# Optimization experiments

Measured on AMD Instinct MI355X. Metric: run time of the kernel, lower is better.

## Reference

```python
import jax, jax.numpy as jnp
import numpy as np

TASK_WEIGHT = 1.0
PHYSICS_WEIGHT = 0.3
HZ = 50.0


def physics_scores(w, hz=HZ):
    """Vectorized port of _score_window_raw. w: [B, T, 3] float. Assumes T >= 20.
    Returns float32 [B] scores in {0, 55..90}."""
    w = jax.lax.stop_gradient(w)  # torch version detaches via .cpu().item()
    B, T, _ = w.shape
    n = T
    mean = jnp.mean(w, axis=1, keepdims=True)          # [B,1,3]
    d = w - mean                                        # centered
    tv = jnp.sum(d * d, axis=(1, 2)) / n                # [B] total (biased) variance
    reject = tv < 0.005
    # per-axis saturation check: too many samples pinned at max |value|
    absw = jnp.abs(w)                                   # [B,T,3]
    max_val = jnp.max(absw, axis=1)                     # [B,3]
    at_max_frac = jnp.mean(jnp.abs(absw - max_val[:, None, :]) < 0.01, axis=1)  # [B,3]
    reject |= jnp.any((max_val >= 0.5) & (at_max_frac > 0.2), axis=1)
    # jerk law (hz >= 50): central-difference twice, p95 of |jerk| pooled over axes
    if hz >= 50:
        dt = 1.0 / hz
        vel = (w[:, 2:, :] - w[:, :-2, :]) / (2 * dt)       # [B, T-2, 3]
        jerk = (vel[:, 2:, :] - vel[:, :-2, :]) / (2 * dt)  # [B, T-4, 3]
        jerks = jnp.abs(jerk).reshape(B, -1)                # [B, 3*(T-4)]
        js = jnp.sort(jerks, axis=1)
        p95_idx = int(jerks.shape[1] * 0.95)                # matches jerks[int(len*0.95)]
        reject |= js[:, p95_idx] > 5000
    # variance-tier score
    s1 = jnp.where(tv > 10.0, 90.0,
         jnp.where(tv > 2.0, 80.0,
         jnp.where(tv > 0.5, 70.0, 58.0)))
    # zero-crossing rate of centered x-axis
    dx = d[:, :, 0]                                      # [B,T]
    zcr = jnp.sum(dx[:, 1:] * dx[:, :-1] < 0, axis=1) / n
    s2 = jnp.where(zcr > 0.15, 85.0, jnp.where(zcr > 0.07, 70.0, 55.0))
    score = jnp.floor((s1 + s2) / 2.0)                   # int() truncation (values positive)
    return jnp.where(reject, 0.0, score).astype(jnp.float32)


def setup_inputs() -> dict:
    key = jax.random.key(0)
    k1, k2, k3 = jax.random.split(key, 3)
    B, T, C = 32768, 512, 128
    predictions = jax.random.normal(k1, (B, C), dtype=jnp.float32)
    labels = jax.random.randint(k2, (B,), 0, C, dtype=jnp.int64)
    # scale accel so physics checks pass with realistic-looking noise (std 0.1 m/s^2)
    imu_windows = 0.1 * jax.random.normal(k3, (B, T, 3), dtype=jnp.float32)
    return {"predictions": predictions, "labels": labels, "imu_windows": imu_windows}


def reference(predictions, labels, imu_windows):
    # task loss: mean cross-entropy
    logp = jax.nn.log_softmax(predictions, axis=-1)                      # [B,C]
    task_loss = -jnp.mean(jnp.take_along_axis(logp, labels[:, None], axis=1)[:, 0])
    # physics penalty
    scores = physics_scores(imu_windows, HZ)                             # [B]
    physics_penalty = jnp.mean(1.0 - scores / 100.0)
    return TASK_WEIGHT * task_loss + PHYSICS_WEIGHT * physics_penalty
```

## Files before the change

kernel.cpp:

```cpp
#include <hip/hip_runtime.h>
#include <math.h>

__device__ __forceinline__ float wave_reduce_sum(float v) {
#pragma unroll
    for (int off = 32; off > 0; off >>= 1) v += __shfl_xor(v, off, 64);
    return v;
}
__device__ __forceinline__ float wave_reduce_max(float v) {
#pragma unroll
    for (int off = 32; off > 0; off >>= 1) v = fmaxf(v, __shfl_xor(v, off, 64));
    return v;
}
__device__ __forceinline__ int wave_reduce_sum_i(int v) {
#pragma unroll
    for (int off = 32; off > 0; off >>= 1) v += __shfl_xor(v, off, 64);
    return v;
}

template <int CT_C>
__global__ void ce_kernel(const float* __restrict__ preds,
                          const int* __restrict__ labels,
                          float* __restrict__ partials, int B, int C_rt) {
    __shared__ float sh[4];
    const int wave = threadIdx.x >> 6, lane = threadIdx.x & 63;
    const int row = blockIdx.x * 4 + wave;
    float loss = 0.f;
    if (row < B) {
        const int C = (CT_C > 0) ? CT_C : C_rt;
        constexpr int NV = (CT_C > 0) ? (CT_C / 64) : 16;
        const int nv = (CT_C > 0) ? NV : ((C_rt + 63) >> 6);
        const float* x = preds + (size_t)row * (size_t)C;
        float vals[NV];
        float m = -3.4e38f;
#pragma unroll
        for (int i = 0; i < NV; i++) {
            if (CT_C == 0 && i >= nv) break;
            const int c = lane + (i << 6);
            float v = (CT_C > 0 || c < C) ? x[c] : -3.4e38f;
            vals[i] = v;
            m = fmaxf(m, v);
        }
        m = wave_reduce_max(m);
        float s = 0.f;
#pragma unroll
        for (int i = 0; i < NV; i++) {
            if (CT_C == 0 && i >= nv) break;
            const int c = lane + (i << 6);
            if (CT_C > 0 || c < C) s += expf(vals[i] - m);
        }
        s = wave_reduce_sum(s);
        const int label = labels[row];
        const int src = label & 63, idx = label >> 6;
        float cand = vals[0];
#pragma unroll
        for (int i = 1; i < NV; i++) {
            if (CT_C == 0 && i >= nv) break;
            if (i == idx) cand = vals[i];
        }
        float xl = __shfl(cand, src, 64);
        loss = logf(s) + m - xl;
    }
    if (lane == 0) sh[wave] = loss;
    __syncthreads();
    if (threadIdx.x == 0) partials[blockIdx.x] = sh[0] + sh[1] + sh[2] + sh[3];
}

template <int CT_T>
__global__ void phys_kernel(const float* __restrict__ wglob,
                            float* __restrict__ partials, int B, int T_rt) {
    extern __shared__ float lds[];
    __shared__ float shScore[4];
    const int wave = threadIdx.x >> 6, lane = threadIdx.x & 63;
    const int row = blockIdx.x * 4 + wave;
    const int T = (CT_T > 0) ? CT_T : T_rt;
    const int N = T * 3;
    float* L = lds + wave * N;
    const bool active = (row < B);

    if (active) {
        const float4* src4 = (const float4*)(wglob + (size_t)row * (size_t)N);
        float4* dst4 = (float4*)L;
        const int n4 = N >> 2;
        for (int i = lane; i < n4; i += 64) dst4[i] = src4[i];
    }
    __syncthreads();

    float score = 0.f;
    if (active) {
        constexpr int KMAX = (CT_T > 0) ? (CT_T + 63) / 64 : 16;
        const int kmax = (CT_T > 0) ? KMAX : ((T_rt + 63) >> 6);
        float v0[KMAX], v1[KMAX], v2[KMAX];
        float sum0 = 0, sum1 = 0, sum2 = 0, sq = 0;
        float mx0 = 0, mx1 = 0, mx2 = 0;
        int jerkcnt = 0;
#pragma unroll
        for (int k = 0; k < KMAX; k++) {
            if (CT_T == 0 && k >= kmax) break;
            const int t = lane + (k << 6);
            float a = 0, b = 0, c = 0;
            if (CT_T > 0 || t < T) { a = L[t * 3 + 0]; b = L[t * 3 + 1]; c = L[t * 3 + 2]; }
            v0[k] = a; v1[k] = b; v2[k] = c;
            sum0 += a; sum1 += b; sum2 += c;
            sq += a * a + b * b + c * c;
            mx0 = fmaxf(mx0, fabsf(a));
            mx1 = fmaxf(mx1, fabsf(b));
            mx2 = fmaxf(mx2, fabsf(c));
            if (t < T - 4) {
                float a2 = L[(t + 2) * 3 + 0], b2 = L[(t + 2) * 3 + 1], c2 = L[(t + 2) * 3 + 2];
                float a4 = L[(t + 4) * 3 + 0], b4 = L[(t + 4) * 3 + 1], c4 = L[(t + 4) * 3 + 2];
                jerkcnt += (fabsf(625.f * (a4 - 2.f * a2 + a)) > 5000.f);
                jerkcnt += (fabsf(625.f * (b4 - 2.f * b2 + b)) > 5000.f);
                jerkcnt += (fabsf(625.f * (c4 - 2.f * c2 + c)) > 5000.f);
            }
        }
        sum0 = wave_reduce_sum(sum0);
        sum1 = wave_reduce_sum(sum1);
        sum2 = wave_reduce_sum(sum2);
        sq   = wave_reduce_sum(sq);
        mx0  = wave_reduce_max(mx0);
        mx1  = wave_reduce_max(mx1);
        mx2  = wave_reduce_max(mx2);
        const float n = (float)T;
        const float m0 = sum0 / n;
        const float tv = (sq - (sum0 * sum0 + sum1 * sum1 + sum2 * sum2) / n) / n;

        int a0 = 0, a1 = 0, a2c = 0, zc = 0;
#pragma unroll
        for (int k = 0; k < KMAX; k++) {
            if (CT_T == 0 && k >= kmax) break;
            const int t = lane + (k << 6);
            if (CT_T > 0 || t < T) {
                a0  += (fabsf(fabsf(v0[k]) - mx0) < 0.01f);
                a1  += (fabsf(fabsf(v1[k]) - mx1) < 0.01f);
                a2c += (fabsf(fabsf(v2[k]) - mx2) < 0.01f);
                if (t < T - 1) {
                    float dxt = v0[k] - m0;
                    float dxn = L[(t + 1) * 3 + 0] - m0;
                    zc += (dxt * dxn < 0.f);
                }
            }
        }
        int pk1 = a0 | (a1 << 10) | (a2c << 20);
        int pk2 = zc | (jerkcnt << 16);
        pk1 = wave_reduce_sum_i(pk1);
        pk2 = wave_reduce_sum_i(pk2);
        a0 = pk1 & 1023; a1 = (pk1 >> 10) & 1023; a2c = (pk1 >> 20) & 1023;
        zc = pk2 & 0xffff; jerkcnt = pk2 >> 16;

        bool reject = (tv < 0.005f);
        const float fT = (float)T;
        if (mx0 >= 0.5f && (a0  / fT) > 0.2f) reject = true;
        if (mx1 >= 0.5f && (a1  / fT) > 0.2f) reject = true;
        if (mx2 >= 0.5f && (a2c / fT) > 0.2f) reject = true;
        const int jtot = (T - 4) * 3;
        const int p95 = (int)((double)jtot * 0.95);
        if (jerkcnt >= jtot - p95) reject = true;

        const float s1 = tv > 10.f ? 90.f : (tv > 2.f ? 80.f : (tv > 0.5f ? 70.f : 58.f));
        const float zcr = zc / fT;
        const float s2 = zcr > 0.15f ? 85.f : (zcr > 0.07f ? 70.f : 55.f);
        score = floorf((s1 + s2) * 0.5f);
        if (reject) score = 0.f;
    }
    if (lane == 0) shScore[wave] = score;
    __syncthreads();
    if (threadIdx.x == 0)
        partials[blockIdx.x] = shScore[0] + shScore[1] + shScore[2] + shScore[3];
}

__global__ void finalize_kernel(const float* __restrict__ p1, const float* __restrict__ p2,
                                int n1, int n2, float* __restrict__ out, int B) {
    __shared__ float sh1[4], sh2[4];
    const int tid = threadIdx.x;
    float s1 = 0.f, s2 = 0.f;
    for (int i = tid; i < n1; i += 256) s1 += p1[i];
    for (int i = tid; i < n2; i += 256) s2 += p2[i];
    s1 = wave_reduce_sum(s1);
    s2 = wave_reduce_sum(s2);
    const int wave = tid >> 6, lane = tid & 63;
    if (lane == 0) { sh1[wave] = s1; sh2[wave] = s2; }
    __syncthreads();
    if (tid == 0) {
        float task = (sh1[0] + sh1[1] + sh1[2] + sh1[3]) / (float)B;
        float pen  = 1.f - (sh2[0] + sh2[1] + sh2[2] + sh2[3]) / (100.f * (float)B);
        out[0] = task + 0.3f * pen;
    }
}

extern "C" void kernel_launch(void* const* d_in, const int* in_sizes, int n_in,
                              void* d_out, int out_size, void* d_ws, size_t ws_size,
                              hipStream_t stream) {
    const float* preds = (const float*)d_in[0];
    const int* labels  = (const int*)d_in[1];
    const float* imu   = (const float*)d_in[2];
    float* out = (float*)d_out;

    const int B = in_sizes[1];
    const int C = in_sizes[0] / B;
    const int T = in_sizes[2] / (3 * B);

    const int ceBlocks = (B + 3) / 4;
    const int phBlocks = (B + 3) / 4;
    float* p1 = (float*)d_ws;
    float* p2 = p1 + ceBlocks;

    if (C == 128) ce_kernel<128><<<ceBlocks, 256, 0, stream>>>(preds, labels, p1, B, C);
    else          ce_kernel<0><<<ceBlocks, 256, 0, stream>>>(preds, labels, p1, B, C);

    const size_t smem = (size_t)4 * (size_t)T * 3 * sizeof(float);
    if (T == 512) phys_kernel<512><<<phBlocks, 256, smem, stream>>>(imu, p2, B, T);
    else          phys_kernel<0><<<phBlocks, 256, smem, stream>>>(imu, p2, B, T);

    finalize_kernel<<<1, 256, 0, stream>>>(p1, p2, ceBlocks, phBlocks, out, B);
}
```

Before: 308.9 us.

## Fuse cross-entropy and physics kernels and use DPP wave reductions

Merges the cross-entropy and physics-score kernels into one launch. Each wave issues its IMU row copy into LDS, computes the cross-entropy loss while that copy is in flight, then scores physics after the barrier. Wave reductions now use DPP row operations plus a readlane in place of shuffle-xor trees. This removes a kernel launch and overlaps the two memory streams, at the cost of higher per-block register pressure from holding both sets of live values.

```diff
diff --git a/kernel.cpp b/kernel.cpp
--- a/kernel.cpp
+++ b/kernel.cpp
@@ -1,31 +1,74 @@
 #include <hip/hip_runtime.h>
 #include <math.h>
 
-__device__ __forceinline__ float wave_reduce_sum(float v) {
-#pragma unroll
-    for (int off = 32; off > 0; off >>= 1) v += __shfl_xor(v, off, 64);
-    return v;
-}
-__device__ __forceinline__ float wave_reduce_max(float v) {
-#pragma unroll
-    for (int off = 32; off > 0; off >>= 1) v = fmaxf(v, __shfl_xor(v, off, 64));
-    return v;
-}
-__device__ __forceinline__ int wave_reduce_sum_i(int v) {
-#pragma unroll
-    for (int off = 32; off > 0; off >>= 1) v += __shfl_xor(v, off, 64);
-    return v;
-}
-
-template <int CT_C>
-__global__ void ce_kernel(const float* __restrict__ preds,
-                          const int* __restrict__ labels,
-                          float* __restrict__ partials, int B, int C_rt) {
-    __shared__ float sh[4];
+template <int CTRL>
+__device__ __forceinline__ float dpp_zero_f(float x) {
+    return __int_as_float(__builtin_amdgcn_update_dpp(
+        0, __float_as_int(x), CTRL, 0xf, 0xf, true));
+}
+template <int CTRL>
+__device__ __forceinline__ float dpp_self_f(float x) {
+    return __int_as_float(__builtin_amdgcn_update_dpp(
+        __float_as_int(x), __float_as_int(x), CTRL, 0xf, 0xf, false));
+}
+template <int CTRL>
+__device__ __forceinline__ int dpp_zero_i(int x) {
+    return __builtin_amdgcn_update_dpp(0, x, CTRL, 0xf, 0xf, true);
+}
+
+__device__ __forceinline__ float dpp_sum_f(float x) {
+    x += dpp_zero_f<0x111>(x);
+    x += dpp_zero_f<0x112>(x);
+    x += dpp_zero_f<0x114>(x);
+    x += dpp_zero_f<0x118>(x);
+    x += dpp_zero_f<0x142>(x);
+    x += dpp_zero_f<0x143>(x);
+    return __int_as_float(__builtin_amdgcn_readlane(__float_as_int(x), 63));
+}
+__device__ __forceinline__ float dpp_max_f(float x) {
+    x = fmaxf(x, dpp_self_f<0x111>(x));
+    x = fmaxf(x, dpp_self_f<0x112>(x));
+    x = fmaxf(x, dpp_self_f<0x114>(x));
+    x = fmaxf(x, dpp_self_f<0x118>(x));
+    x = fmaxf(x, dpp_self_f<0x142>(x));
+    x = fmaxf(x, dpp_self_f<0x143>(x));
+    return __int_as_float(__builtin_amdgcn_readlane(__float_as_int(x), 63));
+}
+__device__ __forceinline__ int dpp_sum_i(int x) {
+    x += dpp_zero_i<0x111>(x);
+    x += dpp_zero_i<0x112>(x);
+    x += dpp_zero_i<0x114>(x);
+    x += dpp_zero_i<0x118>(x);
+    x += dpp_zero_i<0x142>(x);
+    x += dpp_zero_i<0x143>(x);
+    return __builtin_amdgcn_readlane(x, 63);
+}
+
+template <int CT_T, int CT_C>
+__global__ void fused_kernel(const float* __restrict__ imu,
+                             const float* __restrict__ preds,
+                             const int* __restrict__ labels,
+                             float* __restrict__ taskP,
+                             float* __restrict__ scoreP,
+                             int B, int T_rt, int C_rt) {
+    extern __shared__ float lds[];
+    __shared__ float shT[4], shS[4];
     const int wave = threadIdx.x >> 6, lane = threadIdx.x & 63;
     const int row = blockIdx.x * 4 + wave;
+    const int T = (CT_T > 0) ? CT_T : T_rt;
+    const int N = T * 3;
+    float* L = lds + wave * N;
+    const bool active = (row < B);
+
+    if (active) {
+        const float4* src4 = (const float4*)(imu + (size_t)row * (size_t)N);
+        float4* dst4 = (float4*)L;
+        const int n4 = N >> 2;
+        for (int i = lane; i < n4; i += 64) dst4[i] = src4[i];
+    }
+
     float loss = 0.f;
-    if (row < B) {
+    if (active) {
         const int C = (CT_C > 0) ? CT_C : C_rt;
         constexpr int NV = (CT_C > 0) ? (CT_C / 64) : 16;
         const int nv = (CT_C > 0) ? NV : ((C_rt + 63) >> 6);
@@ -40,7 +83,7 @@
             vals[i] = v;
             m = fmaxf(m, v);
         }
-        m = wave_reduce_max(m);
+        m = dpp_max_f(m);
         float s = 0.f;
 #pragma unroll
         for (int i = 0; i < NV; i++) {
@@ -48,7 +91,7 @@
             const int c = lane + (i << 6);
             if (CT_C > 0 || c < C) s += expf(vals[i] - m);
         }
-        s = wave_reduce_sum(s);
+        s = dpp_sum_f(s);
         const int label = labels[row];
         const int src = label & 63, idx = label >> 6;
         float cand = vals[0];
@@ -59,29 +102,6 @@
         }
         float xl = __shfl(cand, src, 64);
         loss = logf(s) + m - xl;
-    }
-    if (lane == 0) sh[wave] = loss;
-    __syncthreads();
-    if (threadIdx.x == 0) partials[blockIdx.x] = sh[0] + sh[1] + sh[2] + sh[3];
-}
-
-template <int CT_T>
-__global__ void phys_kernel(const float* __restrict__ wglob,
-                            float* __restrict__ partials, int B, int T_rt) {
-    extern __shared__ float lds[];
-    __shared__ float shScore[4];
-    const int wave = threadIdx.x >> 6, lane = threadIdx.x & 63;
-    const int row = blockIdx.x * 4 + wave;
-    const int T = (CT_T > 0) ? CT_T : T_rt;
-    const int N = T * 3;
-    float* L = lds + wave * N;
-    const bool active = (row < B);
-
-    if (active) {
-        const float4* src4 = (const float4*)(wglob + (size_t)row * (size_t)N);
-        float4* dst4 = (float4*)L;
-        const int n4 = N >> 2;
-        for (int i = lane; i < n4; i += 64) dst4[i] = src4[i];
     }
     __syncthreads();
 
@@ -113,13 +133,13 @@
                 jerkcnt += (fabsf(625.f * (c4 - 2.f * c2 + c)) > 5000.f);
             }
         }
-        sum0 = wave_reduce_sum(sum0);
-        sum1 = wave_reduce_sum(sum1);
-        sum2 = wave_reduce_sum(sum2);
-        sq   = wave_reduce_sum(sq);
-        mx0  = wave_reduce_max(mx0);
-        mx1  = wave_reduce_max(mx1);
-        mx2  = wave_reduce_max(mx2);
+        sum0 = dpp_sum_f(sum0);
+        sum1 = dpp_sum_f(sum1);
+        sum2 = dpp_sum_f(sum2);
+        sq   = dpp_sum_f(sq);
+        mx0  = dpp_max_f(mx0);
+        mx1  = dpp_max_f(mx1);
+        mx2  = dpp_max_f(mx2);
         const float n = (float)T;
         const float m0 = sum0 / n;
         const float tv = (sq - (sum0 * sum0 + sum1 * sum1 + sum2 * sum2) / n) / n;
@@ -142,8 +162,8 @@
         }
         int pk1 = a0 | (a1 << 10) | (a2c << 20);
         int pk2 = zc | (jerkcnt << 16);
-        pk1 = wave_reduce_sum_i(pk1);
-        pk2 = wave_reduce_sum_i(pk2);
+        pk1 = dpp_sum_i(pk1);
+        pk2 = dpp_sum_i(pk2);
         a0 = pk1 & 1023; a1 = (pk1 >> 10) & 1023; a2c = (pk1 >> 20) & 1023;
         zc = pk2 & 0xffff; jerkcnt = pk2 >> 16;
 
@@ -162,10 +182,19 @@
         score = floorf((s1 + s2) * 0.5f);
         if (reject) score = 0.f;
     }
-    if (lane == 0) shScore[wave] = score;
+
+    if (lane == 0) { shT[wave] = loss; shS[wave] = score; }
     __syncthreads();
-    if (threadIdx.x == 0)
-        partials[blockIdx.x] = shScore[0] + shScore[1] + shScore[2] + shScore[3];
+    if (threadIdx.x == 0) {
+        taskP[blockIdx.x]  = shT[0] + shT[1] + shT[2] + shT[3];
+        scoreP[blockIdx.x] = shS[0] + shS[1] + shS[2] + shS[3];
+    }
+}
+
+__device__ __forceinline__ float wave_reduce_sum_shfl(float v) {
+#pragma unroll
+    for (int off = 32; off > 0; off >>= 1) v += __shfl_xor(v, off, 64);
+    return v;
 }
 
 __global__ void finalize_kernel(const float* __restrict__ p1, const float* __restrict__ p2,
@@ -175,8 +204,8 @@
     float s1 = 0.f, s2 = 0.f;
     for (int i = tid; i < n1; i += 256) s1 += p1[i];
     for (int i = tid; i < n2; i += 256) s2 += p2[i];
-    s1 = wave_reduce_sum(s1);
-    s2 = wave_reduce_sum(s2);
+    s1 = wave_reduce_sum_shfl(s1);
+    s2 = wave_reduce_sum_shfl(s2);
     const int wave = tid >> 6, lane = tid & 63;
     if (lane == 0) { sh1[wave] = s1; sh2[wave] = s2; }
     __syncthreads();
@@ -199,17 +228,15 @@
     const int C = in_sizes[0] / B;
     const int T = in_sizes[2] / (3 * B);
 
-    const int ceBlocks = (B + 3) / 4;
-    const int phBlocks = (B + 3) / 4;
+    const int blocks = (B + 3) / 4;
     float* p1 = (float*)d_ws;
-    float* p2 = p1 + ceBlocks;
-
-    if (C == 128) ce_kernel<128><<<ceBlocks, 256, 0, stream>>>(preds, labels, p1, B, C);
-    else          ce_kernel<0><<<ceBlocks, 256, 0, stream>>>(preds, labels, p1, B, C);
+    float* p2 = p1 + blocks;
 
     const size_t smem = (size_t)4 * (size_t)T * 3 * sizeof(float);
-    if (T == 512) phys_kernel<512><<<phBlocks, 256, smem, stream>>>(imu, p2, B, T);
-    else          phys_kernel<0><<<phBlocks, 256, smem, stream>>>(imu, p2, B, T);
-
-    finalize_kernel<<<1, 256, 0, stream>>>(p1, p2, ceBlocks, phBlocks, out, B);
-}
+    if (T == 512 && C == 128)
+        fused_kernel<512, 128><<<blocks, 256, smem, stream>>>(imu, preds, labels, p1, p2, B, T, C);
+    else
+        fused_kernel<0, 0><<<blocks, 256, smem, stream>>>(imu, preds, labels, p1, p2, B, T, C);
+
+    finalize_kernel<<<1, 256, 0, stream>>>(p1, p2, blocks, blocks, out, B);
+}
```

Result: no change. 304.9 us (-1.3%).
